# Optimization experiments

Measured on AMD Instinct MI355X. Metric: run time of the kernel, lower is better.

The kernel has to match this reference:

```python
import jax, jax.numpy as jnp
import numpy as np

# db4 analysis filters (pywt.Wavelet('db4').dec_lo / dec_hi)
_DEC_LO = np.array([-0.010597401784997278, 0.032883011666982945, 0.030841381835986965,
                    -0.18703481171888114, -0.02798376941698385, 0.6308807679295904,
                    0.7148465705525415, 0.23037781330885523], dtype=np.float32)
_DEC_HI = np.array([-0.23037781330885523, 0.7148465705525415, -0.6308807679295904,
                    -0.02798376941698385, 0.18703481171888114, 0.030841381835986965,
                    -0.032883011666982945, -0.010597401784997278], dtype=np.float32)
# pytorch_wavelets stores filters reversed (torch conv = correlation); lax.conv is
# also correlation, so use the same reversed filters. Shape [2, 1, L].
_H = jnp.asarray(np.stack([_DEC_LO[::-1], _DEC_HI[::-1]])[:, None, :])

B, SW, SWS, HW, K, J = 2048, 4, 64, 8, 128, 3
DWT_LEN = 84  # 14 (lo, level 3) + 35 (hi1) + 21 (hi2) + 14 (hi3)


def _dwt_level(x, h):
    """One analysis level, mode='reflect' (pytorch_wavelets afb1d). x: [M, N]."""
    N = x.shape[-1]
    L = h.shape[-1]
    outsize = (N + L - 1) // 2          # pywt.dwt_coeff_len, non-periodization
    p = 2 * (outsize - 1) - N + L
    if p % 2 == 1:                       # odd total pad: one extra zero at the end
        x = jnp.pad(x, ((0, 0), (0, 1)))
    x = jnp.pad(x, ((0, 0), (p // 2, p // 2)), mode='reflect')
    y = jax.lax.conv_general_dilated(x[:, None, :], h, (2,), 'VALID')  # [M, 2, out]
    return y[:, 0, :], y[:, 1, :]


def setup_inputs() -> dict:
    key = jax.random.key(0)
    k1, k2, k3 = jax.random.split(key, 3)
    x = jax.random.normal(k1, (B, 1, SW * SWS, HW, HW), dtype=jnp.float32)
    # one Conv3d(1 -> K, kernel=(DWT_LEN, 8, 8)) per subwindow, kaiming-ish init
    fan_in = DWT_LEN * HW * HW
    conv_weight = jax.random.normal(k2, (SW, K, DWT_LEN, HW, HW), dtype=jnp.float32) / np.sqrt(fan_in)
    conv_bias = jax.random.normal(k3, (SW, K), dtype=jnp.float32) * 0.01
    return {"x": x, "conv_weight": conv_weight, "conv_bias": conv_bias}


def reference(x, conv_weight, conv_bias):
    b = x.shape[0]
    # [B,1,T,8,8] -> [B,SW,8,8,SWS]: DWT runs along the time axis of each subwindow
    xt = x[:, 0].reshape(b, SW, SWS, HW, HW).transpose(0, 1, 3, 4, 2)
    xm = xt.reshape(-1, SWS)  # [B*SW*64, 64]
    lo, highs = xm, []
    for _ in range(J):
        lo, hi = _dwt_level(lo, _H)
        highs.append(hi)
    coeffs = jnp.concatenate([lo] + highs, axis=-1)  # [M, 84], order: lo, hi1, hi2, hi3
    c = coeffs.reshape(b, SW, HW, HW, DWT_LEN).transpose(0, 1, 4, 2, 3)  # [B,SW,84,8,8]
    # per-subwindow Conv3d that fully reduces (t,h,w) -> [B, SW, K]
    feat = jnp.einsum('bsthw,skthw->bsk', c, conv_weight) + conv_bias[None]
    # Dropout3d is identity in eval; LeakyReLU default slope 0.01 (typo in source
    # means leakyrelu_negative_slope is never applied)
    return jax.nn.leaky_relu(feat, 0.01).reshape(b, SW * K)
```

## Files before the change

kernel.cpp:

```cpp
#include <hip/hip_runtime.h>
#include <stdint.h>

typedef unsigned int   u32;
typedef unsigned short u16;
typedef __bf16 bf16x8 __attribute__((ext_vector_type(8)));
typedef float  f32x4  __attribute__((ext_vector_type(4)));

struct WdT { float v[84][64]; };

constexpr WdT build_wd() {
    WdT W{};
    const float GLc[8] = { 0.23037781330885523f,  0.7148465705525415f,
                           0.6308807679295904f,  -0.02798376941698385f,
                          -0.18703481171888114f,  0.030841381835986965f,
                           0.032883011666982945f,-0.010597401784997278f };
    const float GHc[8] = {-0.010597401784997278f,-0.032883011666982945f,
                           0.030841381835986965f, 0.18703481171888114f,
                          -0.02798376941698385f, -0.6308807679295904f,
                           0.7148465705525415f,  -0.23037781330885523f };
    for (int j = 0; j < 64; ++j) {
        float lo1[35] = {}, lo2[21] = {};
        for (int i = 0; i < 35; ++i) {
            float sl = 0.f, sh = 0.f;
            for (int t = 0; t < 8; ++t) {
                int s = 2*i + t - 6;
                if (s < 0)   s = -s;
                if (s >= 64) s = 126 - s;
                if (s == j) { sl += GLc[t]; sh += GHc[t]; }
            }
            lo1[i] = sl; W.v[14 + i][j] = sh;
        }
        for (int i = 0; i < 21; ++i) {
            float sl = 0.f, sh = 0.f;
            for (int t = 0; t < 8; ++t) {
                int s = 2*i + t - 6;
                if (s < 0)   s = -s;
                if (s >= 36) s = 70 - s;
                if (s < 35) { sl += lo1[s]*GLc[t]; sh += lo1[s]*GHc[t]; }
            }
            lo2[i] = sl; W.v[49 + i][j] = sh;
        }
        for (int i = 0; i < 14; ++i) {
            float sl = 0.f, sh = 0.f;
            for (int t = 0; t < 8; ++t) {
                int s = 2*i + t - 6;
                if (s < 0)   s = -s;
                if (s >= 22) s = 42 - s;
                if (s < 21) { sl += lo2[s]*GLc[t]; sh += lo2[s]*GHc[t]; }
            }
            W.v[i][j] = sl; W.v[70 + i][j] = sh;
        }
    }
    return W;
}

__constant__ WdT WD = build_wd();

__device__ inline u16 f32_bf16(float f) {
    u32 u = __float_as_uint(f);
    u += 0x7fffu + ((u >> 16) & 1u);
    return (u16)(u >> 16);
}
__device__ inline u32 pack2_bf16(float a, float b) {
    u32 ua = __float_as_uint(a); ua += 0x7fffu + ((ua >> 16) & 1u);
    u32 ub = __float_as_uint(b); ub += 0x7fffu + ((ub >> 16) & 1u);
    return (ua >> 16) | (ub & 0xffff0000u);
}

__global__ __launch_bounds__(256) void fold_w(const float* __restrict__ cw,
                                              u16* __restrict__ Wf) {
    const int tid = threadIdx.x;
    const int sk  = blockIdx.x;
    const int s   = sk >> 7;
    const int n   = sk & 127;
    const int hw  = tid & 63;
    const int tg  = __builtin_amdgcn_readfirstlane((int)(tid >> 6));
    const int t0  = tg * 16;
    const float* wk = cw + (size_t)sk * (84 * 64);

    float acc[16];
#pragma unroll
    for (int j = 0; j < 16; ++j) acc[j] = 0.f;

#pragma unroll 4
    for (int tau = 0; tau < 84; ++tau) {
        const float wv = wk[tau * 64 + hw];
#pragma unroll
        for (int j = 0; j < 16; ++j) acc[j] += wv * WD.v[tau][t0 + j];
    }

    const int nt  = n >> 4;
    const int fr  = n & 15;
    const int fq  = (hw >> 3) & 3;
    const int jj  = hw & 7;
    const int kbh = hw >> 5;
#pragma unroll
    for (int j = 0; j < 16; ++j) {
        const int t = t0 + j;
        const size_t idx =
            ((((size_t)(s * 8 + nt)) * 128 + t * 2 + kbh) * 64 + fq * 16 + fr) * 8 + jj;
        Wf[idx] = f32_bf16(acc[j]);
    }
}

__global__ __launch_bounds__(512, 4) void gemm_f(const float* __restrict__ X,
                                                 const u16* __restrict__ Wf,
                                                 const float* __restrict__ bias,
                                                 float* __restrict__ out) {
    __shared__ __align__(16) float R[16 * 132];
    const int tid  = threadIdx.x;
    const int lane = tid & 63;
    const int w    = tid >> 6;
    const int s    = blockIdx.x >> 7;
    const int mt   = blockIdx.x & 127;
    const int fr   = lane & 15;
    const int fq   = lane >> 4;
    const int kb0  = w * 16;

    for (int i = tid; i < 16 * 132; i += 512) R[i] = 0.f;

    const float* xg = X + (size_t)(mt * 16 + fr) * 16384 + s * 4096 + kb0 * 32 + fq * 8;
    const u16*   wg = Wf + ((size_t)(s * 8) * 128 + kb0) * 512 + lane * 8;

    f32x4 acc[8];
#pragma unroll
    for (int nt = 0; nt < 8; ++nt) acc[nt] = (f32x4){0.f, 0.f, 0.f, 0.f};

    f32x4 a0 = __builtin_nontemporal_load(reinterpret_cast<const f32x4*>(xg));
    f32x4 a1 = __builtin_nontemporal_load(reinterpret_cast<const f32x4*>(xg) + 1);

    __syncthreads();

#pragma unroll 2
    for (int kb = 0; kb < 16; ++kb) {
        union { u32 u[4]; bf16x8 v; } av;
        av.u[0] = pack2_bf16(a0.x, a0.y); av.u[1] = pack2_bf16(a0.z, a0.w);
        av.u[2] = pack2_bf16(a1.x, a1.y); av.u[3] = pack2_bf16(a1.z, a1.w);
        const int kn = (kb + 1 < 16) ? kb + 1 : kb;
        a0 = __builtin_nontemporal_load(reinterpret_cast<const f32x4*>(xg + (size_t)kn * 32));
        a1 = __builtin_nontemporal_load(reinterpret_cast<const f32x4*>(xg + (size_t)kn * 32) + 1);
        const u16* wb = wg + (size_t)kb * 512;
#pragma unroll
        for (int nt = 0; nt < 8; ++nt) {
            bf16x8 bf = *reinterpret_cast<const bf16x8*>(wb + (size_t)nt * 65536);
            acc[nt] = __builtin_amdgcn_mfma_f32_16x16x32_bf16(av.v, bf, acc[nt], 0, 0, 0);
        }
    }

#pragma unroll
    for (int nt = 0; nt < 8; ++nt)
#pragma unroll
        for (int r = 0; r < 4; ++r)
            atomicAdd(&R[(fq * 4 + r) * 132 + nt * 16 + fr], acc[nt][r]);
    __syncthreads();

    {
        const int o   = tid * 4;
        const int row = o >> 7;
        const int col = o & 127;
        f32x4 v = *reinterpret_cast<const f32x4*>(&R[row * 132 + col]);
        const f32x4 b = *reinterpret_cast<const f32x4*>(bias + s * 128 + col);
        f32x4 u = v + b;
        u.x = u.x > 0.f ? u.x : 0.01f * u.x;
        u.y = u.y > 0.f ? u.y : 0.01f * u.y;
        u.z = u.z > 0.f ? u.z : 0.01f * u.z;
        u.w = u.w > 0.f ? u.w : 0.01f * u.w;
        __builtin_nontemporal_store(
            u, reinterpret_cast<f32x4*>(out + (size_t)(mt * 16 + row) * 512 + s * 128 + col));
    }
}

extern "C" void kernel_launch(void* const* d_in, const int* in_sizes, int n_in,
                              void* d_out, int out_size, void* d_ws, size_t ws_size,
                              hipStream_t stream) {
    const float* x  = (const float*)d_in[0];
    const float* cw = (const float*)d_in[1];
    const float* cb = (const float*)d_in[2];
    float* out = (float*)d_out;

    u16* Wf = (u16*)d_ws;

    fold_w<<<512, 256, 0, stream>>>(cw, Wf);
    gemm_f<<<512, 512, 0, stream>>>(x, Wf, cb, out);
}
```

Baseline: 272.4 us.

## Relayout folded weights, swizzle block order, and double-buffer GEMM operand loads

Changes the folded-weight layout so the 8 N-tiles of one k-block sit next to each other, which makes each warp's weight loads contiguous. Remaps block IDs so neighbouring workgroups share subwindow weights, aiming for better cache locality. Adds register double-buffering: the X loads run two k-steps ahead and the weight loads one step ahead, with the loop fully unrolled. This hides load latency behind the MFMAs at the cost of more registers, which could reduce occupancy under the 512x4 launch bound.

```diff
diff --git a/kernel.cpp b/kernel.cpp
--- a/kernel.cpp
+++ b/kernel.cpp
@@ -98,7 +98,7 @@
     for (int j = 0; j < 16; ++j) {
         const int t = t0 + j;
         const size_t idx =
-            ((((size_t)(s * 8 + nt)) * 128 + t * 2 + kbh) * 64 + fq * 16 + fr) * 8 + jj;
+            ((((size_t)(s * 128 + t * 2 + kbh)) * 8 + nt) * 64 + fq * 16 + fr) * 8 + jj;
         Wf[idx] = f32_bf16(acc[j]);
     }
 }
@@ -111,40 +111,58 @@
     const int tid  = threadIdx.x;
     const int lane = tid & 63;
     const int w    = tid >> 6;
-    const int s    = blockIdx.x >> 7;
-    const int mt   = blockIdx.x & 127;
+    const int bid  = blockIdx.x;
+    const int wgid = ((bid & 7) << 6) + (bid >> 3);
+    const int s    = wgid >> 7;
+    const int mt   = wgid & 127;
     const int fr   = lane & 15;
     const int fq   = lane >> 4;
     const int kb0  = w * 16;
 
     for (int i = tid; i < 16 * 132; i += 512) R[i] = 0.f;
+    __syncthreads();
 
     const float* xg = X + (size_t)(mt * 16 + fr) * 16384 + s * 4096 + kb0 * 32 + fq * 8;
-    const u16*   wg = Wf + ((size_t)(s * 8) * 128 + kb0) * 512 + lane * 8;
+    const f32x4* xa = reinterpret_cast<const f32x4*>(xg);
+    const u16*   wg = Wf + (size_t)(s * 128 + kb0) * 8 * 512 + lane * 8;
 
     f32x4 acc[8];
 #pragma unroll
     for (int nt = 0; nt < 8; ++nt) acc[nt] = (f32x4){0.f, 0.f, 0.f, 0.f};
 
-    f32x4 a0 = __builtin_nontemporal_load(reinterpret_cast<const f32x4*>(xg));
-    f32x4 a1 = __builtin_nontemporal_load(reinterpret_cast<const f32x4*>(xg) + 1);
-
-    __syncthreads();
-
-#pragma unroll 2
+    f32x4  abuf[2][2];
+    bf16x8 bbuf[2][8];
+
+    abuf[0][0] = __builtin_nontemporal_load(xa + 0);
+    abuf[0][1] = __builtin_nontemporal_load(xa + 1);
+    abuf[1][0] = __builtin_nontemporal_load(xa + 8);
+    abuf[1][1] = __builtin_nontemporal_load(xa + 9);
+#pragma unroll
+    for (int nt = 0; nt < 8; ++nt)
+        bbuf[0][nt] = *reinterpret_cast<const bf16x8*>(wg + nt * 512);
+
+#pragma unroll
     for (int kb = 0; kb < 16; ++kb) {
+        const int cur = kb & 1, nxt = cur ^ 1;
+        if (kb + 1 < 16) {
+            const u16* wb = wg + (size_t)(kb + 1) * 4096;
+#pragma unroll
+            for (int nt = 0; nt < 8; ++nt)
+                bbuf[nxt][nt] = *reinterpret_cast<const bf16x8*>(wb + nt * 512);
+        }
         union { u32 u[4]; bf16x8 v; } av;
-        av.u[0] = pack2_bf16(a0.x, a0.y); av.u[1] = pack2_bf16(a0.z, a0.w);
-        av.u[2] = pack2_bf16(a1.x, a1.y); av.u[3] = pack2_bf16(a1.z, a1.w);
-        const int kn = (kb + 1 < 16) ? kb + 1 : kb;
-        a0 = __builtin_nontemporal_load(reinterpret_cast<const f32x4*>(xg + (size_t)kn * 32));
-        a1 = __builtin_nontemporal_load(reinterpret_cast<const f32x4*>(xg + (size_t)kn * 32) + 1);
-        const u16* wb = wg + (size_t)kb * 512;
-#pragma unroll
-        for (int nt = 0; nt < 8; ++nt) {
-            bf16x8 bf = *reinterpret_cast<const bf16x8*>(wb + (size_t)nt * 65536);
-            acc[nt] = __builtin_amdgcn_mfma_f32_16x16x32_bf16(av.v, bf, acc[nt], 0, 0, 0);
-        }
+        av.u[0] = pack2_bf16(abuf[cur][0].x, abuf[cur][0].y);
+        av.u[1] = pack2_bf16(abuf[cur][0].z, abuf[cur][0].w);
+        av.u[2] = pack2_bf16(abuf[cur][1].x, abuf[cur][1].y);
+        av.u[3] = pack2_bf16(abuf[cur][1].z, abuf[cur][1].w);
+        if (kb + 2 < 16) {
+            abuf[cur][0] = __builtin_nontemporal_load(xa + (kb + 2) * 8);
+            abuf[cur][1] = __builtin_nontemporal_load(xa + (kb + 2) * 8 + 1);
+        }
+#pragma unroll
+        for (int nt = 0; nt < 8; ++nt)
+            acc[nt] = __builtin_amdgcn_mfma_f32_16x16x32_bf16(av.v, bbuf[cur][nt],
+                                                              acc[nt], 0, 0, 0);
     }
 
 #pragma unroll
```

Result: slower. 284.2 us (+4.3%).

## Split GEMM output columns across two blocks with XCD-aware block remap

Applied to the files above, without the earlier changes.

Each GEMM workgroup now computes half of the 128 output channels, which doubles the grid to 1024 blocks and halves accumulator and LDS reduction size. Block IDs are remapped so that consecutive blocks on the same XCD share inputs, and the folded weight layout is reordered so the kb-major tiles for one half are contiguous. The explicit register prefetch of X is replaced by a fully unrolled loop with plain loads. In exchange, each X tile is read twice from memory (once per half), and the occupancy target rises to 8.

```diff
diff --git a/kernel.cpp b/kernel.cpp
--- a/kernel.cpp
+++ b/kernel.cpp
@@ -5,6 +5,7 @@
 typedef unsigned short u16;
 typedef __bf16 bf16x8 __attribute__((ext_vector_type(8)));
 typedef float  f32x4  __attribute__((ext_vector_type(4)));
+typedef float  f32x2  __attribute__((ext_vector_type(2)));
 
 struct WdT { float v[84][64]; };
 
@@ -98,75 +99,72 @@
     for (int j = 0; j < 16; ++j) {
         const int t = t0 + j;
         const size_t idx =
-            ((((size_t)(s * 8 + nt)) * 128 + t * 2 + kbh) * 64 + fq * 16 + fr) * 8 + jj;
+            ((((size_t)(s * 128 + t * 2 + kbh)) * 8 + nt) * 64 + fq * 16 + fr) * 8 + jj;
         Wf[idx] = f32_bf16(acc[j]);
     }
 }
 
-__global__ __launch_bounds__(512, 4) void gemm_f(const float* __restrict__ X,
+__global__ __launch_bounds__(512, 8) void gemm_f(const float* __restrict__ X,
                                                  const u16* __restrict__ Wf,
                                                  const float* __restrict__ bias,
                                                  float* __restrict__ out) {
-    __shared__ __align__(16) float R[16 * 132];
+    __shared__ __align__(16) float R[16 * 68];
     const int tid  = threadIdx.x;
     const int lane = tid & 63;
     const int w    = tid >> 6;
-    const int s    = blockIdx.x >> 7;
-    const int mt   = blockIdx.x & 127;
+    const int bid  = blockIdx.x;
+    const int wgid = ((bid & 7) << 7) + (bid >> 3);
+    const int nh   = wgid & 1;
+    const int mt   = (wgid >> 1) & 127;
+    const int s    = wgid >> 8;
     const int fr   = lane & 15;
     const int fq   = lane >> 4;
     const int kb0  = w * 16;
 
-    for (int i = tid; i < 16 * 132; i += 512) R[i] = 0.f;
+    for (int i = tid; i < 16 * 68; i += 512) R[i] = 0.f;
+    __syncthreads();
 
     const float* xg = X + (size_t)(mt * 16 + fr) * 16384 + s * 4096 + kb0 * 32 + fq * 8;
-    const u16*   wg = Wf + ((size_t)(s * 8) * 128 + kb0) * 512 + lane * 8;
+    const f32x4* xa = reinterpret_cast<const f32x4*>(xg);
+    const u16*   wg = Wf + ((size_t)(s * 128 + kb0) * 8 + nh * 4) * 512 + lane * 8;
 
-    f32x4 acc[8];
+    f32x4 acc[4];
 #pragma unroll
-    for (int nt = 0; nt < 8; ++nt) acc[nt] = (f32x4){0.f, 0.f, 0.f, 0.f};
+    for (int nt = 0; nt < 4; ++nt) acc[nt] = (f32x4){0.f, 0.f, 0.f, 0.f};
 
-    f32x4 a0 = __builtin_nontemporal_load(reinterpret_cast<const f32x4*>(xg));
-    f32x4 a1 = __builtin_nontemporal_load(reinterpret_cast<const f32x4*>(xg) + 1);
-
-    __syncthreads();
-
-#pragma unroll 2
+#pragma unroll
     for (int kb = 0; kb < 16; ++kb) {
+        const f32x4 a0 = xa[kb * 8];
+        const f32x4 a1 = xa[kb * 8 + 1];
         union { u32 u[4]; bf16x8 v; } av;
         av.u[0] = pack2_bf16(a0.x, a0.y); av.u[1] = pack2_bf16(a0.z, a0.w);
         av.u[2] = pack2_bf16(a1.x, a1.y); av.u[3] = pack2_bf16(a1.z, a1.w);
-        const int kn = (kb + 1 < 16) ? kb + 1 : kb;
-        a0 = __builtin_nontemporal_load(reinterpret_cast<const f32x4*>(xg + (size_t)kn * 32));
-        a1 = __builtin_nontemporal_load(reinterpret_cast<const f32x4*>(xg + (size_t)kn * 32) + 1);
-        const u16* wb = wg + (size_t)kb * 512;
+        const u16* wb = wg + (size_t)kb * 4096;
 #pragma unroll
-        for (int nt = 0; nt < 8; ++nt) {
-            bf16x8 bf = *reinterpret_cast<const bf16x8*>(wb + (size_t)nt * 65536);
+        for (int nt = 0; nt < 4; ++nt) {
+            const bf16x8 bf = *reinterpret_cast<const bf16x8*>(wb + nt * 512);
             acc[nt] = __builtin_amdgcn_mfma_f32_16x16x32_bf16(av.v, bf, acc[nt], 0, 0, 0);
         }
     }
 
 #pragma unroll
-    for (int nt = 0; nt < 8; ++nt)
+    for (int nt = 0; nt < 4; ++nt)
 #pragma unroll
         for (int r = 0; r < 4; ++r)
-            atomicAdd(&R[(fq * 4 + r) * 132 + nt * 16 + fr], acc[nt][r]);
+            atomicAdd(&R[(fq * 4 + r) * 68 + nt * 16 + fr], acc[nt][r]);
     __syncthreads();
 
     {
-        const int o   = tid * 4;
-        const int row = o >> 7;
-        const int col = o & 127;
-        f32x4 v = *reinterpret_cast<const f32x4*>(&R[row * 132 + col]);
-        const f32x4 b = *reinterpret_cast<const f32x4*>(bias + s * 128 + col);
-        f32x4 u = v + b;
+        const int o     = tid * 2;
+        const int row   = o >> 6;
+        const int col64 = o & 63;
+        const f32x2 v = *reinterpret_cast<const f32x2*>(&R[row * 68 + col64]);
+        const f32x2 b = *reinterpret_cast<const f32x2*>(bias + s * 128 + nh * 64 + col64);
+        f32x2 u = v + b;
         u.x = u.x > 0.f ? u.x : 0.01f * u.x;
         u.y = u.y > 0.f ? u.y : 0.01f * u.y;
-        u.z = u.z > 0.f ? u.z : 0.01f * u.z;
-        u.w = u.w > 0.f ? u.w : 0.01f * u.w;
-        __builtin_nontemporal_store(
-            u, reinterpret_cast<f32x4*>(out + (size_t)(mt * 16 + row) * 512 + s * 128 + col));
+        *reinterpret_cast<f32x2*>(
+            out + (size_t)(mt * 16 + row) * 512 + s * 128 + nh * 64 + col64) = u;
     }
 }
 
@@ -181,5 +179,5 @@
     u16* Wf = (u16*)d_ws;
 
     fold_w<<<512, 256, 0, stream>>>(cw, Wf);
-    gemm_f<<<512, 512, 0, stream>>>(x, Wf, cb, out);
+    gemm_f<<<1024, 512, 0, stream>>>(x, Wf, cb, out);
 }
```

After: 258.0 us. -5.3%, faster.

## Stage X and W tiles through LDS with async double-buffered loads, split N across waves

Applied to the files above, without the earlier changes.

The GEMM kernel now copies X and folded-weight tiles into shared memory with global_load_lds in a double-buffered pipeline. Each wave owns one 16-column output slice instead of a K-slice, which removes the shared-memory atomic reduction. The weight layout in fold_w is reordered so each K step is one contiguous block, and the block index is remapped for locality. In exchange it adds per-step barriers, a large LDS footprint that may lower occupancy, and swizzled A reads.

```diff
diff --git a/kernel.cpp b/kernel.cpp
--- a/kernel.cpp
+++ b/kernel.cpp
@@ -67,6 +67,12 @@
     return (ua >> 16) | (ub & 0xffff0000u);
 }
 
+typedef const __attribute__((address_space(1))) u32 gas_u32;
+typedef __attribute__((address_space(3)))       u32 las_u32;
+__device__ inline void gl16(const void* g, void* l) {
+    __builtin_amdgcn_global_load_lds((gas_u32*)g, (las_u32*)l, 16, 0, 0);
+}
+
 __global__ __launch_bounds__(256) void fold_w(const float* __restrict__ cw,
                                               u16* __restrict__ Wf) {
     const int tid = threadIdx.x;
@@ -98,7 +104,7 @@
     for (int j = 0; j < 16; ++j) {
         const int t = t0 + j;
         const size_t idx =
-            ((((size_t)(s * 8 + nt)) * 128 + t * 2 + kbh) * 64 + fq * 16 + fr) * 8 + jj;
+            ((((size_t)(s * 128 + t * 2 + kbh)) * 8 + nt) * 64 + fq * 16 + fr) * 8 + jj;
         Wf[idx] = f32_bf16(acc[j]);
     }
 }
@@ -107,66 +113,80 @@
                                                  const u16* __restrict__ Wf,
                                                  const float* __restrict__ bias,
                                                  float* __restrict__ out) {
-    __shared__ __align__(16) float R[16 * 132];
+    __shared__ float As[2][2048];
+    __shared__ u16   Bs[2][16384];
+
     const int tid  = threadIdx.x;
     const int lane = tid & 63;
     const int w    = tid >> 6;
-    const int s    = blockIdx.x >> 7;
-    const int mt   = blockIdx.x & 127;
     const int fr   = lane & 15;
     const int fq   = lane >> 4;
-    const int kb0  = w * 16;
-
-    for (int i = tid; i < 16 * 132; i += 512) R[i] = 0.f;
-
-    const float* xg = X + (size_t)(mt * 16 + fr) * 16384 + s * 4096 + kb0 * 32 + fq * 8;
-    const u16*   wg = Wf + ((size_t)(s * 8) * 128 + kb0) * 512 + lane * 8;
-
-    f32x4 acc[8];
-#pragma unroll
-    for (int nt = 0; nt < 8; ++nt) acc[nt] = (f32x4){0.f, 0.f, 0.f, 0.f};
-
-    f32x4 a0 = __builtin_nontemporal_load(reinterpret_cast<const f32x4*>(xg));
-    f32x4 a1 = __builtin_nontemporal_load(reinterpret_cast<const f32x4*>(xg) + 1);
-
-    __syncthreads();
-
+
+    const int bid  = blockIdx.x;
+    const int wg   = ((bid & 7) << 6) + (bid >> 3);
+    const int mt   = wg & 127;
+    const int s    = wg >> 7;
+
+    const int am   = tid >> 5;
+    const int acb  = ((tid & 31) * 16) ^ ((am & 7) << 4);
+    const float* xa = X + (size_t)(mt * 16 + am) * 16384 + s * 4096 + (acb >> 2);
+    const char* wb0 = (const char*)Wf + ((size_t)s << 20) + (size_t)tid * 16;
+
+    f32x4 acc = (f32x4){0.f, 0.f, 0.f, 0.f};
+
+#define STAGE(buf, st)                                                         \
+    do {                                                                       \
+        gl16(xa + (size_t)(st) * 128, (char*)&As[buf][0] + tid * 16);          \
+        const char* gb = wb0 + ((size_t)(st) << 15);                           \
+        char*       lb = (char*)&Bs[buf][0] + tid * 16;                        \
+        gl16(gb,         lb);                                                  \
+        gl16(gb +  8192, lb +  8192);                                          \
+        gl16(gb + 16384, lb + 16384);                                          \
+        gl16(gb + 24576, lb + 24576);                                          \
+    } while (0)
+
+    STAGE(0, 0);
+
+    const int swz = (fr & 7) << 4;
 #pragma unroll 2
-    for (int kb = 0; kb < 16; ++kb) {
-        union { u32 u[4]; bf16x8 v; } av;
-        av.u[0] = pack2_bf16(a0.x, a0.y); av.u[1] = pack2_bf16(a0.z, a0.w);
-        av.u[2] = pack2_bf16(a1.x, a1.y); av.u[3] = pack2_bf16(a1.z, a1.w);
-        const int kn = (kb + 1 < 16) ? kb + 1 : kb;
-        a0 = __builtin_nontemporal_load(reinterpret_cast<const f32x4*>(xg + (size_t)kn * 32));
-        a1 = __builtin_nontemporal_load(reinterpret_cast<const f32x4*>(xg + (size_t)kn * 32) + 1);
-        const u16* wb = wg + (size_t)kb * 512;
-#pragma unroll
-        for (int nt = 0; nt < 8; ++nt) {
-            bf16x8 bf = *reinterpret_cast<const bf16x8*>(wb + (size_t)nt * 65536);
-            acc[nt] = __builtin_amdgcn_mfma_f32_16x16x32_bf16(av.v, bf, acc[nt], 0, 0, 0);
-        }
-    }
-
-#pragma unroll
-    for (int nt = 0; nt < 8; ++nt)
-#pragma unroll
-        for (int r = 0; r < 4; ++r)
-            atomicAdd(&R[(fq * 4 + r) * 132 + nt * 16 + fr], acc[nt][r]);
-    __syncthreads();
-
-    {
-        const int o   = tid * 4;
-        const int row = o >> 7;
-        const int col = o & 127;
-        f32x4 v = *reinterpret_cast<const f32x4*>(&R[row * 132 + col]);
-        const f32x4 b = *reinterpret_cast<const f32x4*>(bias + s * 128 + col);
-        f32x4 u = v + b;
-        u.x = u.x > 0.f ? u.x : 0.01f * u.x;
-        u.y = u.y > 0.f ? u.y : 0.01f * u.y;
-        u.z = u.z > 0.f ? u.z : 0.01f * u.z;
-        u.w = u.w > 0.f ? u.w : 0.01f * u.w;
-        __builtin_nontemporal_store(
-            u, reinterpret_cast<f32x4*>(out + (size_t)(mt * 16 + row) * 512 + s * 128 + col));
+    for (int step = 0; step < 32; ++step) {
+        const int buf = step & 1;
+        if (step + 1 < 32) {
+            STAGE(buf ^ 1, step + 1);
+            asm volatile("s_waitcnt vmcnt(5)" ::: "memory");
+        } else {
+            asm volatile("s_waitcnt vmcnt(0)" ::: "memory");
+        }
+        __builtin_amdgcn_s_barrier();
+
+        const char* Ab = (const char*)&As[buf][0];
+        const u16*  Bb = &Bs[buf][0];
+#pragma unroll
+        for (int sub = 0; sub < 4; ++sub) {
+            const bf16x8 bf = *reinterpret_cast<const bf16x8*>(
+                Bb + ((sub * 8 + w) * 64 + lane) * 8);
+            const int b0 = (sub * 128 + fq * 32) ^ swz;
+            const int b1 = (sub * 128 + fq * 32 + 16) ^ swz;
+            const f32x4 r0 = *reinterpret_cast<const f32x4*>(Ab + fr * 512 + b0);
+            const f32x4 r1 = *reinterpret_cast<const f32x4*>(Ab + fr * 512 + b1);
+            union { u32 u[4]; bf16x8 v; } av;
+            av.u[0] = pack2_bf16(r0.x, r0.y); av.u[1] = pack2_bf16(r0.z, r0.w);
+            av.u[2] = pack2_bf16(r1.x, r1.y); av.u[3] = pack2_bf16(r1.z, r1.w);
+            acc = __builtin_amdgcn_mfma_f32_16x16x32_bf16(av.v, bf, acc, 0, 0, 0);
+        }
+
+        asm volatile("s_waitcnt lgkmcnt(0)" ::: "memory");
+        __builtin_amdgcn_s_barrier();
+    }
+#undef STAGE
+
+    const float bb = bias[s * 128 + w * 16 + fr];
+    float* og = out + (size_t)(mt * 16) * 512 + s * 128 + w * 16 + fr;
+#pragma unroll
+    for (int r = 0; r < 4; ++r) {
+        float v = acc[r] + bb;
+        v = v > 0.f ? v : 0.01f * v;
+        og[(size_t)(fq * 4 + r) * 512] = v;
     }
 }
 
```

After: 231.4 us. 1.18x faster.
